# Performance work log

Hardware: AMD Instinct MI355X
Metric: run time of the kernel (lower is better)

## Reference

```python
import jax, jax.numpy as jnp
import numpy as np

N_LIG, N_PROT, K = 1024, 8192, 48
N = N_LIG + N_PROT
HID, FEAT, DEPTH = 256, 32, 5
NF = 6                      # sinusoid frequencies -> 12-dim distance embedding
EDGE_DIM = 4 * NF           # per-block dist emb (12) + top-level dist emb (12)
NORM = 5.0                  # agg_norm_factor
_FREQS = (2.0 * np.pi * 4.0 ** np.arange(NF) / 15.0).astype(np.float32)

def sin_emb(d2):
    # d2: [E,1] squared distances -> [E, 2*NF] sinusoidal embedding
    d = jnp.sqrt(d2 + 1e-8)
    x = d * _FREQS
    return jnp.concatenate([jnp.sin(x), jnp.cos(x)], axis=-1)

def knn_edges(coors):
    # KNN (k=48, no self loops) restricted to ligand query nodes (first N_LIG),
    # matching edges[:, :N_lig*k] slicing of knn_graph(flow='target_to_source').
    c = jax.lax.stop_gradient(coors)
    lig = c[:N_LIG]
    d2 = jnp.sum((lig[:, None, :] - c[None, :, :]) ** 2, axis=-1)  # [N_LIG, N]
    d2 = d2.at[jnp.arange(N_LIG), jnp.arange(N_LIG)].set(jnp.inf)
    _, idx = jax.lax.top_k(-d2, K)                                  # [N_LIG, K]
    row = jnp.repeat(jnp.arange(N_LIG), K)
    col = idx.reshape(-1)
    return row, col

def egnn(h, x, row, col, W_in, b_in, W_out, b_out, edge_W1, edge_b1, edge_W2, edge_b2, att_W, att_b, node_W1, node_b1, node_W2, node_b2, coord_W1, coord_b1, coord_W2, coord_b2, coord_W3):
    # EDM-style EGNN: per block 1 GCL (edge MLP + attention gate + node MLP residual)
    # followed by an equivariant coordinate update; sin distance embedding.
    emb0 = sin_emb(jnp.sum((x[row] - x[col]) ** 2, axis=-1, keepdims=True))
    h = h @ W_in + b_in
    for l in range(DEPTH):
        diff = x[row] - x[col]                         # [E,3]
        d2 = jnp.sum(diff ** 2, axis=-1, keepdims=True)
        cdiff = diff / (jnp.sqrt(d2 + 1e-8) + 1.0)     # norm_constant = 1
        ea = jnp.concatenate([sin_emb(d2), emb0], axis=-1)  # [E, EDGE_DIM]
        m = jax.nn.silu(jnp.concatenate([h[row], h[col], ea], axis=-1) @ edge_W1[l] + edge_b1[l])
        m = jax.nn.silu(m @ edge_W2[l] + edge_b2[l])
        m = m * jax.nn.sigmoid(m @ att_W[l] + att_b[l])         # attention gate
        agg = jax.ops.segment_sum(m, row, num_segments=N) / NORM
        u = jax.nn.silu(jnp.concatenate([h, agg], axis=-1) @ node_W1[l] + node_b1[l])
        h = h + (u @ node_W2[l] + node_b2[l])                    # residual node update
        c = jax.nn.silu(jnp.concatenate([h[row], h[col], ea], axis=-1) @ coord_W1[l] + coord_b1[l])  # use_latest_h
        c = jax.nn.silu(c @ coord_W2[l] + coord_b2[l])
        x = x + jax.ops.segment_sum(cdiff * (c @ coord_W3[l]), row, num_segments=N) / NORM
    return h @ W_out + b_out, x

def setup_inputs():
    key = jax.random.key(0)
    ks = jax.random.split(key, 24)
    f32 = jnp.float32
    def nrm(i, shape, scale=0.05):
        return jax.random.normal(ks[i], shape, dtype=f32) * scale
    return {
        'protein_positions': nrm(0, (N_PROT, 3), 3.0),
        'protein_ele': jax.random.randint(ks[1], (N_PROT,), 0, 5),
        'protein_amino_acid': jax.random.randint(ks[2], (N_PROT,), 0, 20),
        'protein_is_backbone': jax.random.randint(ks[3], (N_PROT,), 0, 2),
        'Xt_pos': nrm(4, (N_LIG, 3), 1.0),
        'Xt_features': nrm(5, (N_LIG, FEAT), 1.0),
        't': jax.random.randint(ks[6], (N_LIG,), 0, 1000),
        'Wt_time': nrm(7, (1000, 8), 1.0),
        'W_ele': nrm(8, (5, 16), 1.0),
        'W_aa': nrm(9, (20, 16), 1.0),
        'W_bb': nrm(10, (2, 8), 1.0),
        'W_in': nrm(11, (40, HID)), 'b_in': jnp.zeros((HID,), f32),
        'W_out': nrm(12, (HID, FEAT)), 'b_out': jnp.zeros((FEAT,), f32),
        'edge_W1': nrm(13, (DEPTH, 2 * HID + EDGE_DIM, HID)), 'edge_b1': jnp.zeros((DEPTH, HID), f32),
        'edge_W2': nrm(14, (DEPTH, HID, HID)), 'edge_b2': jnp.zeros((DEPTH, HID), f32),
        'att_W': nrm(15, (DEPTH, HID, 1)), 'att_b': jnp.zeros((DEPTH, 1), f32),
        'node_W1': nrm(16, (DEPTH, 2 * HID, HID)), 'node_b1': jnp.zeros((DEPTH, HID), f32),
        'node_W2': nrm(17, (DEPTH, HID, HID)), 'node_b2': jnp.zeros((DEPTH, HID), f32),
        'coord_W1': nrm(18, (DEPTH, 2 * HID + EDGE_DIM, HID)), 'coord_b1': jnp.zeros((DEPTH, HID), f32),
        'coord_W2': nrm(19, (DEPTH, HID, HID)), 'coord_b2': jnp.zeros((DEPTH, HID), f32),
        'coord_W3': nrm(20, (DEPTH, HID, 1), 0.001),
        'pos_w': jnp.ones((1, 1), f32),
    }

def reference(protein_positions, protein_ele, protein_amino_acid, protein_is_backbone, Xt_pos, Xt_features, t, Wt_time, W_ele, W_aa, W_bb, W_in, b_in, W_out, b_out, edge_W1, edge_b1, edge_W2, edge_b2, att_W, att_b, node_W1, node_b1, node_W2, node_b2, coord_W1, coord_b1, coord_W2, coord_b2, coord_W3, pos_w):
    prot_feat = jnp.concatenate([W_ele[protein_ele], W_aa[protein_amino_acid], W_bb[protein_is_backbone]], axis=-1)  # [N_PROT,40]
    feats = jnp.concatenate([jnp.concatenate([Xt_features, Wt_time[t]], axis=-1), prot_feat], axis=0)  # [N,40]
    coors = jnp.concatenate([Xt_pos, protein_positions], axis=0)  # [N,3]
    row, col = knn_edges(coors)
    h, x = egnn(feats, coors, row, col, W_in, b_in, W_out, b_out, edge_W1, edge_b1, edge_W2, edge_b2, att_W, att_b, node_W1, node_b1, node_W2, node_b2, coord_W1, coord_b1, coord_W2, coord_b2, coord_W3)
    # pos_linear: Linear(1,1,bias=False) applied elementwise == scalar multiply
    return x[:N_LIG] * pos_w[0, 0], h[:N_LIG]
```

## Files before the change

kernel.cpp:

```cpp
#include <hip/hip_runtime.h>
#include <hip/hip_bf16.h>
#include <math.h>

#define N_LIGC 1024
#define NTOT 9216
#define KNN 48
#define HID 256
#define DEPTHC 5
#define ETOT (N_LIGC*KNN)
#define KBINS 4096
#define PACK_BLKS 1484

typedef unsigned short u16;
typedef __attribute__((ext_vector_type(8))) short bf16x8;
typedef __attribute__((ext_vector_type(4))) float f32x4;

__device__ __forceinline__ float freq_f(int i){
  double p = (double)(1 << (2*i));
  return (float)((2.0*3.14159265358979323846)*p/15.0);
}
__device__ __forceinline__ float silu_f(float v){
  return v*__builtin_amdgcn_rcpf(1.0f+__expf(-v));
}
__device__ __forceinline__ float sigm_f(float v){
// ... 169 lines not shown
        aR[0][0]=__builtin_amdgcn_mfma_f32_16x16x32_bf16(a0,b0,aR[0][0],0,0,0);
        aR[0][1]=__builtin_amdgcn_mfma_f32_16x16x32_bf16(a0,b1,aR[0][1],0,0,0);
        aR[1][0]=__builtin_amdgcn_mfma_f32_16x16x32_bf16(a1,b0,aR[1][0],0,0,0);
        aR[1][1]=__builtin_amdgcn_mfma_f32_16x16x32_bf16(a1,b1,aR[1][1],0,0,0);
        aR[2][0]=__builtin_amdgcn_mfma_f32_16x16x32_bf16(a2,b0,aR[2][0],0,0,0);
        aR[2][1]=__builtin_amdgcn_mfma_f32_16x16x32_bf16(a2,b1,aR[2][1],0,0,0);
      }
      #pragma unroll
      for (int mt=0;mt<3;mt++)
      #pragma unroll
      for (int nt=0;nt<2;nt++){
        int n = wv*32 + nt*16 + nl;
        #pragma unroll
        for (int r=0;r<4;r++){
          int m = mt*16 + quad*4 + r;
          int node = base + m;
          if (m < 36 && node < N_LIGC) R[(size_t)node*HID + n] = aR[mt][nt][r];
        }
      }
    }
    return;
  }
  if (tid >= 256) return;
  unsigned int* hist  = (unsigned int*)smem;
  int*          candI = (int*)(smem + 16384);
  float*        candV = (float*)(smem + 20480);
  unsigned int* scanb = (unsigned int*)(smem + 24576);
  float*        selD  = (float*)(smem + 25600);
  int*          sInt  = (int*)(smem + 25792);
  int b = blockIdx.x - 256;
  for (int i=tid;i<KBINS;i+=256) hist[i]=0u;
  if (tid==0){ sInt[3]=0; }
  float px = X[b*3+0], py = X[b*3+1], pz = X[b*3+2];
  __syncthreads();
  float d2v[36];
  float mn = INFINITY;
  #pragma unroll
  for (int j=0;j<36;j++){
    int i = tid + 256*j;
    float dx = __fsub_rn(px, X[i*3+0]);
    float dy = __fsub_rn(py, X[i*3+1]);
    float dz = __fsub_rn(pz, X[i*3+2]);
    float d2 = __fadd_rn(__fadd_rn(__fmul_rn(dx,dx),__fmul_rn(dy,dy)),__fmul_rn(dz,dz));
    if (i==b) d2 = INFINITY;
    d2v[j] = d2;
    mn = fminf(mn, d2);
  }
  {
    unsigned mkey = __float_as_uint(mn) >> 19;
    if (mkey >= KBINS) mkey = KBINS-1;
    atomicAdd(&hist[mkey], 1u);
  }
  __syncthreads();
  unsigned s=0;
  {
    #pragma unroll 4
    for (int k=0;k<16;k++) s += hist[tid*16+k];
    scanb[tid]=s;
  }
  __syncthreads();
  #pragma unroll
  for (int off=1; off<256; off<<=1){
    unsigned v = (tid>=off) ? scanb[tid-off] : 0u;
    __syncthreads();
    scanb[tid] += v;
    __syncthreads();
  }
  {
    unsigned incl = scanb[tid];
    unsigned excl = incl - s;
    if (excl < (unsigned)KNN && incl >= (unsigned)KNN){ sInt[2] = tid; sInt[1] = (int)excl; }
  }
  __syncthreads();
  if (tid==0){
    unsigned c = (unsigned)sInt[1]; int bin = sInt[2]*16;
    for (;;bin++){
      unsigned hh = hist[bin];
      if (c + hh >= (unsigned)KNN) break;
      c += hh;
    }
    sInt[0] = bin;
  }
  __syncthreads();
  int Bp = sInt[0];
  #pragma unroll
  for (int j=0;j<36;j++){
    float d2 = d2v[j];
    int key = (int)(__float_as_uint(d2) >> 19);
    if (key <= Bp){
      int c = atomicAdd(&sInt[3], 1);
      if (c < 1024){ candI[c] = tid + 256*j; candV[c] = d2; }
    }
  }
  __syncthreads();
  {
    int m = sInt[3]; if (m > 1024) m = 1024;
    for (int c = tid; c < m; c += 256){
      float v = candV[c]; int idx = candI[c];
      int rank = 0;
      for (int o = 0; o < m; o++){
        float ov = candV[o];
        if (ov < v || (ov == v && candI[o] < idx)) rank++;
      }
      if (rank < KNN){ col[b*KNN+rank] = idx; selD[rank] = v; }
    }
  }
  __syncthreads();
  if (tid < KNN){
    float d = sqrtf(selD[tid] + 1e-8f);
    int base = (b*KNN+tid)*12;
    #pragma unroll
    for (int i=0;i<6;i++){
      float fr = freq_f(i);
      emb0[base+i]   = f2b_p(sinf(d*fr));
      emb0[base+6+i] = f2b_p(cosf(d*fr));
    }
  }
}

__global__ __launch_bounds__(256,4) void k_comb_edge(
    const u16* __restrict__ Qb, const float* __restrict__ R,
    const float* __restrict__ xc,
    const int* __restrict__ colIdx, const u16* __restrict__ emb0,
    const u16* __restrict__ W1cP, const float* __restrict__ B1,
    const u16* __restrict__ W2p, const float* __restrict__ B2,
    const float* __restrict__ attW, const float* __restrict__ attB,
    u16* __restrict__ agg_bf, int l)
{
  __shared__ __align__(16) u16 sQ[48*264];
  __shared__ __align__(16) u16 sEA[48*40];
  __shared__ float sR[256];
  __shared__ int sCol[48];
  __shared__ float sD[48];
  __shared__ float sSig[48];
  __shared__ float sDot[48][4];

  int row = blockIdx.x, tid = threadIdx.x;
  int lane = tid & 63, ng = tid >> 6;
  int quad = lane >> 4, nl = lane & 15;

  if (tid < 48) sCol[tid] = colIdx[(size_t)row*KNN + tid];
  sR[tid] = R[(size_t)row*HID + tid];
  __syncthreads();
  for (int t = tid; t < 48*32; t += 256){
    int e = t >> 5, q = t & 31;
    uint4 v = ((const uint4*)(Qb + (size_t)sCol[e]*HID))[q];
    *(uint4*)(sQ + e*264 + q*8) = v;
  }
  if (tid < 48){
    int cg = sCol[tid];
    float dx = xc[row*3+0]-xc[cg*3+0];
    float dy = xc[row*3+1]-xc[cg*3+1];
    float dz = xc[row*3+2]-xc[cg*3+2];
    float d = sqrtf(dx*dx+dy*dy+dz*dz + 1e-8f);
    sD[tid] = d;
    const unsigned int* ep = (const unsigned int*)(emb0 + ((size_t)row*KNN + tid)*12);
    unsigned int* dd = (unsigned int*)(sEA + tid*40 + 12);
    #pragma unroll
    for (int i=0;i<6;i++) dd[i] = ep[i];
    u16* ea = sEA + tid*40;
    #pragma unroll
    for (int i=24;i<32;i++) ea[i] = 0;
  }
  __syncthreads();
  for (int t=tid; t<288; t+=256){
    int e = t/6, i = t - 6*e;
    float fr = 0.41887903f * (float)(1 << (2*i));
    float x = sD[e]*fr;
    u16* ea = sEA + e*40;
    ea[i]   = f2b(__sinf(x));
    ea[6+i] = f2b(__cosf(x));
  }
  __syncthreads();

  f32x4 zero4 = {0.f,0.f,0.f,0.f};
  f32x4 acc[3][4];
  #pragma unroll
  for (int i=0;i<3;i++){ acc[i][0]=zero4; acc[i][1]=zero4; acc[i][2]=zero4; acc[i][3]=zero4; }
  {
    const u16* Wc = W1cP + (size_t)l*32*HID;
    const u16* wb = Wc + ((size_t)(ng*4)*64 + lane)*8;
    bf16x8 b0 = *(const bf16x8*)(wb);
    bf16x8 b1 = *(const bf16x8*)(wb + 512);
    bf16x8 b2 = *(const bf16x8*)(wb + 1024);
    bf16x8 b3 = *(const bf16x8*)(wb + 1536);
    bf16x8 a0 = *(const bf16x8*)(sEA + (0*16+nl)*40 + quad*8);
    bf16x8 a1 = *(const bf16x8*)(sEA + (1*16+nl)*40 + quad*8);
    bf16x8 a2 = *(const bf16x8*)(sEA + (2*16+nl)*40 + quad*8);
    acc[0][0]=__builtin_amdgcn_mfma_f32_16x16x32_bf16(a0,b0,acc[0][0],0,0,0);
    acc[0][1]=__builtin_amdgcn_mfma_f32_16x16x32_bf16(a0,b1,acc[0][1],0,0,0);
    acc[0][2]=__builtin_amdgcn_mfma_f32_16x16x32_bf16(a0,b2,acc[0][2],0,0,0);
    acc[0][3]=__builtin_amdgcn_mfma_f32_16x16x32_bf16(a0,b3,acc[0][3],0,0,0);
    acc[1][0]=__builtin_amdgcn_mfma_f32_16x16x32_bf16(a1,b0,acc[1][0],0,0,0);
    acc[1][1]=__builtin_amdgcn_mfma_f32_16x16x32_bf16(a1,b1,acc[1][1],0,0,0);
    acc[1][2]=__builtin_amdgcn_mfma_f32_16x16x32_bf16(a1,b2,acc[1][2],0,0,0);
    acc[1][3]=__builtin_amdgcn_mfma_f32_16x16x32_bf16(a1,b3,acc[1][3],0,0,0);
    acc[2][0]=__builtin_amdgcn_mfma_f32_16x16x32_bf16(a2,b0,acc[2][0],0,0,0);
    acc[2][1]=__builtin_amdgcn_mfma_f32_16x16x32_bf16(a2,b1,acc[2][1],0,0,0);
    acc[2][2]=__builtin_amdgcn_mfma_f32_16x16x32_bf16(a2,b2,acc[2][2],0,0,0);
    acc[2][3]=__builtin_amdgcn_mfma_f32_16x16x32_bf16(a2,b3,acc[2][3],0,0,0);
  }
  #pragma unroll
  for (int mt=0;mt<3;mt++)
  #pragma unroll
  for (int nt=0;nt<4;nt++){
    int n = ng*64 + nt*16 + nl;
    float bb = B1[l*HID + n] + sR[n];
    #pragma unroll
    for (int r=0;r<4;r++){
      int m = mt*16 + quad*4 + r;
      float v = acc[mt][nt][r] + bb + b2f(sQ[m*264 + n]);
      sQ[m*264 + n] = f2b(silu_f(v));
    }
  }
  __syncthreads();

  f32x4 acc2[3][4];
  #pragma unroll
  for (int i=0;i<3;i++){ acc2[i][0]=zero4; acc2[i][1]=zero4; acc2[i][2]=zero4; acc2[i][3]=zero4; }
  const u16* W2 = W2p + (size_t)l*HID*HID;
  #pragma unroll 2
  for (int k0=0;k0<8;k0++){
    bf16x8 a0 = *(const bf16x8*)(sQ + (0*16+nl)*264 + k0*32 + quad*8);
    bf16x8 a1 = *(const bf16x8*)(sQ + (1*16+nl)*264 + k0*32 + quad*8);
    bf16x8 a2 = *(const bf16x8*)(sQ + (2*16+nl)*264 + k0*32 + quad*8);
    const u16* wb = W2 + ((size_t)(k0*16 + ng*4)*64 + lane)*8;
    bf16x8 b0 = *(const bf16x8*)(wb);
    bf16x8 b1 = *(const bf16x8*)(wb + 512);
    bf16x8 b2 = *(const bf16x8*)(wb + 1024);
    bf16x8 b3 = *(const bf16x8*)(wb + 1536);
    acc2[0][0]=__builtin_amdgcn_mfma_f32_16x16x32_bf16(a0,b0,acc2[0][0],0,0,0);
    acc2[0][1]=__builtin_amdgcn_mfma_f32_16x16x32_bf16(a0,b1,acc2[0][1],0,0,0);
    acc2[0][2]=__builtin_amdgcn_mfma_f32_16x16x32_bf16(a0,b2,acc2[0][2],0,0,0);
    acc2[0][3]=__builtin_amdgcn_mfma_f32_16x16x32_bf16(a0,b3,acc2[0][3],0,0,0);
    acc2[1][0]=__builtin_amdgcn_mfma_f32_16x16x32_bf16(a1,b0,acc2[1][0],0,0,0);
    acc2[1][1]=__builtin_amdgcn_mfma_f32_16x16x32_bf16(a1,b1,acc2[1][1],0,0,0);
    acc2[1][2]=__builtin_amdgcn_mfma_f32_16x16x32_bf16(a1,b2,acc2[1][2],0,0,0);
    acc2[1][3]=__builtin_amdgcn_mfma_f32_16x16x32_bf16(a1,b3,acc2[1][3],0,0,0);
    acc2[2][0]=__builtin_amdgcn_mfma_f32_16x16x32_bf16(a2,b0,acc2[2][0],0,0,0);
    acc2[2][1]=__builtin_amdgcn_mfma_f32_16x16x32_bf16(a2,b1,acc2[2][1],0,0,0);
    acc2[2][2]=__builtin_amdgcn_mfma_f32_16x16x32_bf16(a2,b2,acc2[2][2],0,0,0);
    acc2[2][3]=__builtin_amdgcn_mfma_f32_16x16x32_bf16(a2,b3,acc2[2][3],0,0,0);
  }
  float aw[4], bb2[4];
  #pragma unroll
  for (int nt=0;nt<4;nt++){
    int n = ng*64 + nt*16 + nl;
    aw[nt]  = attW[l*HID + n];
    bb2[nt] = B2[l*HID + n];
  }
  float dotp[3][4];
  #pragma unroll
  for (int mt=0;mt<3;mt++){
    #pragma unroll
    for (int r=0;r<4;r++) dotp[mt][r] = 0.f;
    #pragma unroll
    for (int nt=0;nt<4;nt++){
      #pragma unroll
      for (int r=0;r<4;r++){
        float s = silu_f(acc2[mt][nt][r] + bb2[nt]);
        acc2[mt][nt][r] = s;
        dotp[mt][r] += s*aw[nt];
      }
    }
  }
  #pragma unroll
  for (int off=1; off<16; off<<=1){
    #pragma unroll
    for (int mt=0;mt<3;mt++)
    #pragma unroll
    for (int r=0;r<4;r++)
      dotp[mt][r] += __shfl_xor(dotp[mt][r], off);
  }
  if (nl == 0){
    #pragma unroll
    for (int mt=0;mt<3;mt++)
    #pragma unroll
    for (int r=0;r<4;r++)
      sDot[mt*16 + quad*4 + r][ng] = dotp[mt][r];
  }
  __syncthreads();
  if (tid < 48) sSig[tid] = sigm_f(sDot[tid][0]+sDot[tid][1]+sDot[tid][2]+sDot[tid][3] + attB[l]);
  __syncthreads();
  float sgv[3][4];
  #pragma unroll
  for (int mt=0;mt<3;mt++)
  #pragma unroll
  for (int r=0;r<4;r++)
    sgv[mt][r] = sSig[mt*16 + quad*4 + r];
  #pragma unroll
  for (int nt=0;nt<4;nt++){
    float a = 0.f;
    #pragma unroll
    for (int mt=0;mt<3;mt++)
    #pragma unroll
    for (int r=0;r<4;r++)
      a += acc2[mt][nt][r]*sgv[mt][r];
    a += __shfl_xor(a, 16);
    a += __shfl_xor(a, 32);
    if (quad == 0) agg_bf[(size_t)row*HID + ng*64 + nt*16 + nl] = f2b(a*0.2f);
  }
}

__global__ __launch_bounds__(512,1) void k_node(
    float* __restrict__ h,
    const u16* __restrict__ agg_bf,
    const u16* __restrict__ W1p, const float* __restrict__ B1,
    const u16* __restrict__ W2p, const float* __restrict__ B2,
    const u16* __restrict__ cWab, u16* __restrict__ QbC, float* __restrict__ RC,
    const u16* __restrict__ eWabN, u16* __restrict__ QbE, float* __restrict__ RE, int doE,
    const u16* __restrict__ WoutP, const float* __restrict__ bout,
    float* __restrict__ outH, int doOut, int l)
{
  __shared__ __align__(16) u16 sA[48*520];
  __shared__ __align__(16) u16 sU[48*264];
  u16* sH = sA;
  int blk=blockIdx.x, tid=threadIdx.x;
  int lane=tid&63, wv=tid>>6, quad=lane>>4, nl=lane&15;
  int base = blk*36;
  for (int t=tid; t<48*64; t+=512){
    int i=t>>6, s=t&63;
    unsigned int lo, hi;
    if (i < 36){
      float4 hv = ((const float4*)(h + (size_t)(base+i)*HID))[s];
      lo = (unsigned int)f2b(hv.x) | ((unsigned int)f2b(hv.y) << 16);
      hi = (unsigned int)f2b(hv.z) | ((unsigned int)f2b(hv.w) << 16);
    } else { lo = 0u; hi = 0u; }
    uint2 ov; ov.x = lo; ov.y = hi;
    *(uint2*)(sA + i*520 + s*4) = ov;
  }
  for (int t=tid; t<48*32; t+=512){
    int i=t>>5, q=t&31;
    uint4 v;
    int node = base+i;
    if (i < 36 && node < N_LIGC) v = ((const uint4*)(agg_bf + (size_t)node*HID))[q];
    else { v.x=0u; v.y=0u; v.z=0u; v.w=0u; }
    *(uint4*)(sA + i*520 + 256 + q*8) = v;
  }
  __syncthreads();
  f32x4 zero4 = {0.f,0.f,0.f,0.f};
  f32x4 acc[3][2];
  #pragma unroll
  for (int i=0;i<3;i++){ acc[i][0]=zero4; acc[i][1]=zero4; }
  const u16* Wp = W1p + (size_t)l*512*HID;
  #pragma unroll 2
  for (int k0=0;k0<16;k0++){
    bf16x8 a0 = *(const bf16x8*)(sA + (0*16+nl)*520 + k0*32 + quad*8);
    bf16x8 a1 = *(const bf16x8*)(sA + (1*16+nl)*520 + k0*32 + quad*8);
    bf16x8 a2 = *(const bf16x8*)(sA + (2*16+nl)*520 + k0*32 + quad*8);
    const u16* wb = Wp + ((size_t)(k0*16 + wv*2)*64 + lane)*8;
    bf16x8 b0 = *(const bf16x8*)(wb);
    bf16x8 b1 = *(const bf16x8*)(wb + 512);
    acc[0][0]=__builtin_amdgcn_mfma_f32_16x16x32_bf16(a0,b0,acc[0][0],0,0,0);
    acc[0][1]=__builtin_amdgcn_mfma_f32_16x16x32_bf16(a0,b1,acc[0][1],0,0,0);
    acc[1][0]=__builtin_amdgcn_mfma_f32_16x16x32_bf16(a1,b0,acc[1][0],0,0,0);
    acc[1][1]=__builtin_amdgcn_mfma_f32_16x16x32_bf16(a1,b1,acc[1][1],0,0,0);
    acc[2][0]=__builtin_amdgcn_mfma_f32_16x16x32_bf16(a2,b0,acc[2][0],0,0,0);
    acc[2][1]=__builtin_amdgcn_mfma_f32_16x16x32_bf16(a2,b1,acc[2][1],0,0,0);
  }
  #pragma unroll
  for (int mt=0;mt<3;mt++)
  #pragma unroll
  for (int nt=0;nt<2;nt++){
    int n = wv*32 + nt*16 + nl;
    float bb = B1[l*HID + n];
    #pragma unroll
    for (int r=0;r<4;r++){
      int m = mt*16 + quad*4 + r;
      sU[m*264 + n] = f2b(silu_f(acc[mt][nt][r] + bb));
    }
  }
  __syncthreads();
  f32x4 acc2[3][2];
  #pragma unroll
  for (int i=0;i<3;i++){ acc2[i][0]=zero4; acc2[i][1]=zero4; }
  const u16* W2 = W2p + (size_t)l*HID*HID;
  #pragma unroll 2
  for (int k0=0;k0<8;k0++){
    bf16x8 a0 = *(const bf16x8*)(sU + (0*16+nl)*264 + k0*32 + quad*8);
    bf16x8 a1 = *(const bf16x8*)(sU + (1*16+nl)*264 + k0*32 + quad*8);
    bf16x8 a2 = *(const bf16x8*)(sU + (2*16+nl)*264 + k0*32 + quad*8);
    const u16* wb = W2 + ((size_t)(k0*16 + wv*2)*64 + lane)*8;
    bf16x8 b0 = *(const bf16x8*)(wb);
    bf16x8 b1 = *(const bf16x8*)(wb + 512);
    acc2[0][0]=__builtin_amdgcn_mfma_f32_16x16x32_bf16(a0,b0,acc2[0][0],0,0,0);
    acc2[0][1]=__builtin_amdgcn_mfma_f32_16x16x32_bf16(a0,b1,acc2[0][1],0,0,0);
    acc2[1][0]=__builtin_amdgcn_mfma_f32_16x16x32_bf16(a1,b0,acc2[1][0],0,0,0);
    acc2[1][1]=__builtin_amdgcn_mfma_f32_16x16x32_bf16(a1,b1,acc2[1][1],0,0,0);
    acc2[2][0]=__builtin_amdgcn_mfma_f32_16x16x32_bf16(a2,b0,acc2[2][0],0,0,0);
    acc2[2][1]=__builtin_amdgcn_mfma_f32_16x16x32_bf16(a2,b1,acc2[2][1],0,0,0);
  }
  #pragma unroll
  for (int mt=0;mt<3;mt++)
  #pragma unroll
  for (int nt=0;nt<2;nt++){
    int n = wv*32 + nt*16 + nl;
    float bb = B2[l*HID + n];
    #pragma unroll
    for (int r=0;r<4;r++){
      int m = mt*16 + quad*4 + r;
      if (m < 36){
        size_t idx = (size_t)(base+m)*HID + n;
        float v = h[idx] + acc2[mt][nt][r] + bb;
        h[idx] = v;
        sH[m*264 + n] = f2b(v);
      } else {
        sH[m*264 + n] = 0;
      }
    }
  }
  __syncthreads();

  int isLig = (base < N_LIGC);
  const u16* Wl = cWab + (size_t)l*512*HID;
  {
    f32x4 qc[3][2], qe[3][2];
    #pragma unroll
    for (int i=0;i<3;i++){ qc[i][0]=zero4; qc[i][1]=zero4; qe[i][0]=zero4; qe[i][1]=zero4; }
    #pragma unroll 2
    for (int k0=0;k0<8;k0++){
      bf16x8 a0 = *(const bf16x8*)(sH + (0*16+nl)*264 + k0*32 + quad*8);
      bf16x8 a1 = *(const bf16x8*)(sH + (1*16+nl)*264 + k0*32 + quad*8);
      bf16x8 a2 = *(const bf16x8*)(sH + (2*16+nl)*264 + k0*32 + quad*8);
      const u16* wbC = Wl    + ((size_t)((k0+8)*16 + wv*2)*64 + lane)*8;
      const u16* wbE = eWabN + ((size_t)((k0+8)*16 + wv*2)*64 + lane)*8;
      bf16x8 c0 = *(const bf16x8*)(wbC);
      bf16x8 c1 = *(const bf16x8*)(wbC + 512);
      bf16x8 e0 = *(const bf16x8*)(wbE);
      bf16x8 e1 = *(const bf16x8*)(wbE + 512);
      qc[0][0]=__builtin_amdgcn_mfma_f32_16x16x32_bf16(a0,c0,qc[0][0],0,0,0);
      qc[0][1]=__builtin_amdgcn_mfma_f32_16x16x32_bf16(a0,c1,qc[0][1],0,0,0);
      qc[1][0]=__builtin_amdgcn_mfma_f32_16x16x32_bf16(a1,c0,qc[1][0],0,0,0);
      qc[1][1]=__builtin_amdgcn_mfma_f32_16x16x32_bf16(a1,c1,qc[1][1],0,0,0);
      qc[2][0]=__builtin_amdgcn_mfma_f32_16x16x32_bf16(a2,c0,qc[2][0],0,0,0);
      qc[2][1]=__builtin_amdgcn_mfma_f32_16x16x32_bf16(a2,c1,qc[2][1],0,0,0);
      qe[0][0]=__builtin_amdgcn_mfma_f32_16x16x32_bf16(a0,e0,qe[0][0],0,0,0);
      qe[0][1]=__builtin_amdgcn_mfma_f32_16x16x32_bf16(a0,e1,qe[0][1],0,0,0);
      qe[1][0]=__builtin_amdgcn_mfma_f32_16x16x32_bf16(a1,e0,qe[1][0],0,0,0);
      qe[1][1]=__builtin_amdgcn_mfma_f32_16x16x32_bf16(a1,e1,qe[1][1],0,0,0);
      qe[2][0]=__builtin_amdgcn_mfma_f32_16x16x32_bf16(a2,e0,qe[2][0],0,0,0);
      qe[2][1]=__builtin_amdgcn_mfma_f32_16x16x32_bf16(a2,e1,qe[2][1],0,0,0);
    }
    #pragma unroll
    for (int mt=0;mt<3;mt++)
    #pragma unroll
    for (int nt=0;nt<2;nt++){
      int n = wv*32 + nt*16 + nl;
      #pragma unroll
      for (int r=0;r<4;r++){
        int m = mt*16 + quad*4 + r;
        if (m < 36) QbC[(size_t)(base+m)*HID + n] = f2b(qc[mt][nt][r]);
      }
    }
    if (doE){
      #pragma unroll
      for (int mt=0;mt<3;mt++)
      #pragma unroll
      for (int nt=0;nt<2;nt++){
        int n = wv*32 + nt*16 + nl;
        #pragma unroll
        for (int r=0;r<4;r++){
          int m = mt*16 + quad*4 + r;
          if (m < 36) QbE[(size_t)(base+m)*HID + n] = f2b(qe[mt][nt][r]);
        }
      }
    }
  }
  if (isLig){
    f32x4 rc[3][2], re[3][2];
    #pragma unroll
    for (int i=0;i<3;i++){ rc[i][0]=zero4; rc[i][1]=zero4; re[i][0]=zero4; re[i][1]=zero4; }
    #pragma unroll 2
    for (int k0=0;k0<8;k0++){
      bf16x8 a0 = *(const bf16x8*)(sH + (0*16+nl)*264 + k0*32 + quad*8);
      bf16x8 a1 = *(const bf16x8*)(sH + (1*16+nl)*264 + k0*32 + quad*8);
      bf16x8 a2 = *(const bf16x8*)(sH + (2*16+nl)*264 + k0*32 + quad*8);
      const u16* wbC = Wl    + ((size_t)(k0*16 + wv*2)*64 + lane)*8;
      const u16* wbE = eWabN + ((size_t)(k0*16 + wv*2)*64 + lane)*8;
      bf16x8 c0 = *(const bf16x8*)(wbC);
      bf16x8 c1 = *(const bf16x8*)(wbC + 512);
      bf16x8 e0 = *(const bf16x8*)(wbE);
      bf16x8 e1 = *(const bf16x8*)(wbE + 512);
      rc[0][0]=__builtin_amdgcn_mfma_f32_16x16x32_bf16(a0,c0,rc[0][0],0,0,0);
      rc[0][1]=__builtin_amdgcn_mfma_f32_16x16x32_bf16(a0,c1,rc[0][1],0,0,0);
      rc[1][0]=__builtin_amdgcn_mfma_f32_16x16x32_bf16(a1,c0,rc[1][0],0,0,0);
      rc[1][1]=__builtin_amdgcn_mfma_f32_16x16x32_bf16(a1,c1,rc[1][1],0,0,0);
      rc[2][0]=__builtin_amdgcn_mfma_f32_16x16x32_bf16(a2,c0,rc[2][0],0,0,0);
      rc[2][1]=__builtin_amdgcn_mfma_f32_16x16x32_bf16(a2,c1,rc[2][1],0,0,0);
      re[0][0]=__builtin_amdgcn_mfma_f32_16x16x32_bf16(a0,e0,re[0][0],0,0,0);
      re[0][1]=__builtin_amdgcn_mfma_f32_16x16x32_bf16(a0,e1,re[0][1],0,0,0);
      re[1][0]=__builtin_amdgcn_mfma_f32_16x16x32_bf16(a1,e0,re[1][0],0,0,0);
      re[1][1]=__builtin_amdgcn_mfma_f32_16x16x32_bf16(a1,e1,re[1][1],0,0,0);
      re[2][0]=__builtin_amdgcn_mfma_f32_16x16x32_bf16(a2,e0,re[2][0],0,0,0);
      re[2][1]=__builtin_amdgcn_mfma_f32_16x16x32_bf16(a2,e1,re[2][1],0,0,0);
    }
    #pragma unroll
    for (int mt=0;mt<3;mt++)
    #pragma unroll
    for (int nt=0;nt<2;nt++){
      int n = wv*32 + nt*16 + nl;
      #pragma unroll
      for (int r=0;r<4;r++){
        int m = mt*16 + quad*4 + r;
        int node = base + m;
        if (m < 36 && node < N_LIGC) RC[(size_t)node*HID + n] = rc[mt][nt][r];
      }
    }
    if (doE){
      #pragma unroll
      for (int mt=0;mt<3;mt++)
      #pragma unroll
      for (int nt=0;nt<2;nt++){
        int n = wv*32 + nt*16 + nl;
        #pragma unroll
        for (int r=0;r<4;r++){
          int m = mt*16 + quad*4 + r;
          int node = base + m;
          if (m < 36 && node < N_LIGC) RE[(size_t)node*HID + n] = re[mt][nt][r];
        }
      }
    }
  }
  if (doOut && isLig && wv < 2){
    int ntw = wv;
    f32x4 o[3]; o[0]=zero4; o[1]=zero4; o[2]=zero4;
    #pragma unroll 2
    for (int k0=0;k0<8;k0++){
      bf16x8 b = *(const bf16x8*)(WoutP + ((size_t)(k0*2 + ntw)*64 + lane)*8);
      #pragma unroll
      for (int mt=0;mt<3;mt++){
        bf16x8 a = *(const bf16x8*)(sH + (mt*16+nl)*264 + k0*32 + quad*8);
        o[mt] = __builtin_amdgcn_mfma_f32_16x16x32_bf16(a,b,o[mt],0,0,0);
      }
    }
    int n = ntw*16 + nl;
    float bb = bout[n];
    #pragma unroll
    for (int mt=0;mt<3;mt++)
    #pragma unroll
    for (int r=0;r<4;r++){
      int m = mt*16 + quad*4 + r;
      int node = base + m;
      if (m < 36 && node < N_LIGC)
        outH[(size_t)node*32 + n] = o[mt][r] + bb;
    }
  }
}

__global__ __launch_bounds__(256,4) void k_comb_coord(
    const u16* __restrict__ Qb, const float* __restrict__ R,
    const float* __restrict__ xc, float* __restrict__ xn,
    const int* __restrict__ colIdx, const u16* __restrict__ emb0,
    const u16* __restrict__ W1cP, const float* __restrict__ B1,
    const u16* __restrict__ W2p, const float* __restrict__ B2,
    const float* __restrict__ cW3,
    const float* __restrict__ posw, float* __restrict__ outX, int doOut, int l)
{
  __shared__ __align__(16) u16 sQ[48*264];
  __shared__ __align__(16) u16 sEA[48*40];
  __shared__ float sR[256];
  __shared__ int sCol[48];
  __shared__ float sD[48];
  __shared__ float sCd[48*3];
  __shared__ float sS[48];
  __shared__ float sDot[48][4];

  int row = blockIdx.x, tid = threadIdx.x;
  int lane = tid & 63, ng = tid >> 6;
  int quad = lane >> 4, nl = lane & 15;

  if (tid < 48) sCol[tid] = colIdx[(size_t)row*KNN + tid];
  sR[tid] = R[(size_t)row*HID + tid];
  __syncthreads();
  for (int t = tid; t < 48*32; t += 256){
    int e = t >> 5, q = t & 31;
    uint4 v = ((const uint4*)(Qb + (size_t)sCol[e]*HID))[q];
    *(uint4*)(sQ + e*264 + q*8) = v;
  }
  if (tid < 48){
    int cg = sCol[tid];
    float dx = xc[row*3+0]-xc[cg*3+0];
    float dy = xc[row*3+1]-xc[cg*3+1];
    float dz = xc[row*3+2]-xc[cg*3+2];
    float d = sqrtf(dx*dx+dy*dy+dz*dz + 1e-8f);
    sD[tid] = d;
    float rden = __builtin_amdgcn_rcpf(d + 1.0f);
    sCd[tid*3+0]=dx*rden; sCd[tid*3+1]=dy*rden; sCd[tid*3+2]=dz*rden;
    const unsigned int* ep = (const unsigned int*)(emb0 + ((size_t)row*KNN + tid)*12);
    unsigned int* dd = (unsigned int*)(sEA + tid*40 + 12);
    #pragma unroll
    for (int i=0;i<6;i++) dd[i] = ep[i];
    u16* ea = sEA + tid*40;
    #pragma unroll
    for (int i=24;i<32;i++) ea[i] = 0;
  }
  __syncthreads();
  for (int t=tid; t<288; t+=256){
    int e = t/6, i = t - 6*e;
    float fr = 0.41887903f * (float)(1 << (2*i));
    float x = sD[e]*fr;
    u16* ea = sEA + e*40;
    ea[i]   = f2b(__sinf(x));
    ea[6+i] = f2b(__cosf(x));
  }
  __syncthreads();

  f32x4 zero4 = {0.f,0.f,0.f,0.f};
  f32x4 acc[3][4];
  #pragma unroll
  for (int i=0;i<3;i++){ acc[i][0]=zero4; acc[i][1]=zero4; acc[i][2]=zero4; acc[i][3]=zero4; }
  {
    const u16* Wc = W1cP + (size_t)l*32*HID;
    const u16* wb = Wc + ((size_t)(ng*4)*64 + lane)*8;
    bf16x8 b0 = *(const bf16x8*)(wb);
    bf16x8 b1 = *(const bf16x8*)(wb + 512);
    bf16x8 b2 = *(const bf16x8*)(wb + 1024);
    bf16x8 b3 = *(const bf16x8*)(wb + 1536);
    bf16x8 a0 = *(const bf16x8*)(sEA + (0*16+nl)*40 + quad*8);
    bf16x8 a1 = *(const bf16x8*)(sEA + (1*16+nl)*40 + quad*8);
    bf16x8 a2 = *(const bf16x8*)(sEA + (2*16+nl)*40 + quad*8);
    acc[0][0]=__builtin_amdgcn_mfma_f32_16x16x32_bf16(a0,b0,acc[0][0],0,0,0);
    acc[0][1]=__builtin_amdgcn_mfma_f32_16x16x32_bf16(a0,b1,acc[0][1],0,0,0);
    acc[0][2]=__builtin_amdgcn_mfma_f32_16x16x32_bf16(a0,b2,acc[0][2],0,0,0);
    acc[0][3]=__builtin_amdgcn_mfma_f32_16x16x32_bf16(a0,b3,acc[0][3],0,0,0);
    acc[1][0]=__builtin_amdgcn_mfma_f32_16x16x32_bf16(a1,b0,acc[1][0],0,0,0);
    acc[1][1]=__builtin_amdgcn_mfma_f32_16x16x32_bf16(a1,b1,acc[1][1],0,0,0);
    acc[1][2]=__builtin_amdgcn_mfma_f32_16x16x32_bf16(a1,b2,acc[1][2],0,0,0);
    acc[1][3]=__builtin_amdgcn_mfma_f32_16x16x32_bf16(a1,b3,acc[1][3],0,0,0);
    acc[2][0]=__builtin_amdgcn_mfma_f32_16x16x32_bf16(a2,b0,acc[2][0],0,0,0);
    acc[2][1]=__builtin_amdgcn_mfma_f32_16x16x32_bf16(a2,b1,acc[2][1],0,0,0);
    acc[2][2]=__builtin_amdgcn_mfma_f32_16x16x32_bf16(a2,b2,acc[2][2],0,0,0);
    acc[2][3]=__builtin_amdgcn_mfma_f32_16x16x32_bf16(a2,b3,acc[2][3],0,0,0);
  }
  #pragma unroll
  for (int mt=0;mt<3;mt++)
  #pragma unroll
  for (int nt=0;nt<4;nt++){
    int n = ng*64 + nt*16 + nl;
    float bb = B1[l*HID + n] + sR[n];
    #pragma unroll
    for (int r=0;r<4;r++){
      int m = mt*16 + quad*4 + r;
      float v = acc[mt][nt][r] + bb + b2f(sQ[m*264 + n]);
      sQ[m*264 + n] = f2b(silu_f(v));
    }
  }
  __syncthreads();

  f32x4 acc2[3][4];
  #pragma unroll
  for (int i=0;i<3;i++){ acc2[i][0]=zero4; acc2[i][1]=zero4; acc2[i][2]=zero4; acc2[i][3]=zero4; }
  const u16* W2 = W2p + (size_t)l*HID*HID;
  #pragma unroll 2
  for (int k0=0;k0<8;k0++){
    bf16x8 a0 = *(const bf16x8*)(sQ + (0*16+nl)*264 + k0*32 + quad*8);
    bf16x8 a1 = *(const bf16x8*)(sQ + (1*16+nl)*264 + k0*32 + quad*8);
    bf16x8 a2 = *(const bf16x8*)(sQ + (2*16+nl)*264 + k0*32 + quad*8);
    const u16* wb = W2 + ((size_t)(k0*16 + ng*4)*64 + lane)*8;
    bf16x8 b0 = *(const bf16x8*)(wb);
    bf16x8 b1 = *(const bf16x8*)(wb + 512);
    bf16x8 b2 = *(const bf16x8*)(wb + 1024);
    bf16x8 b3 = *(const bf16x8*)(wb + 1536);
    acc2[0][0]=__builtin_amdgcn_mfma_f32_16x16x32_bf16(a0,b0,acc2[0][0],0,0,0);
    acc2[0][1]=__builtin_amdgcn_mfma_f32_16x16x32_bf16(a0,b1,acc2[0][1],0,0,0);
    acc2[0][2]=__builtin_amdgcn_mfma_f32_16x16x32_bf16(a0,b2,acc2[0][2],0,0,0);
    acc2[0][3]=__builtin_amdgcn_mfma_f32_16x16x32_bf16(a0,b3,acc2[0][3],0,0,0);
    acc2[1][0]=__builtin_amdgcn_mfma_f32_16x16x32_bf16(a1,b0,acc2[1][0],0,0,0);
    acc2[1][1]=__builtin_amdgcn_mfma_f32_16x16x32_bf16(a1,b1,acc2[1][1],0,0,0);
    acc2[1][2]=__builtin_amdgcn_mfma_f32_16x16x32_bf16(a1,b2,acc2[1][2],0,0,0);
    acc2[1][3]=__builtin_amdgcn_mfma_f32_16x16x32_bf16(a1,b3,acc2[1][3],0,0,0);
    acc2[2][0]=__builtin_amdgcn_mfma_f32_16x16x32_bf16(a2,b0,acc2[2][0],0,0,0);
    acc2[2][1]=__builtin_amdgcn_mfma_f32_16x16x32_bf16(a2,b1,acc2[2][1],0,0,0);
    acc2[2][2]=__builtin_amdgcn_mfma_f32_16x16x32_bf16(a2,b2,acc2[2][2],0,0,0);
    acc2[2][3]=__builtin_amdgcn_mfma_f32_16x16x32_bf16(a2,b3,acc2[2][3],0,0,0);
  }
  float cw[4], bb2[4];
  #pragma unroll
  for (int nt=0;nt<4;nt++){
    int n = ng*64 + nt*16 + nl;
    cw[nt]  = cW3[l*HID + n];
    bb2[nt] = B2[l*HID + n];
  }
  float dotp[3][4];
  #pragma unroll
  for (int mt=0;mt<3;mt++){
    #pragma unroll
    for (int r=0;r<4;r++) dotp[mt][r] = 0.f;
    #pragma unroll
    for (int nt=0;nt<4;nt++){
      #pragma unroll
      for (int r=0;r<4;r++){
        float s = silu_f(acc2[mt][nt][r] + bb2[nt]);
        dotp[mt][r] += s*cw[nt];
      }
    }
  }
  #pragma unroll
  for (int off=1; off<16; off<<=1){
    #pragma unroll
    for (int mt=0;mt<3;mt++)
    #pragma unroll
    for (int r=0;r<4;r++)
      dotp[mt][r] += __shfl_xor(dotp[mt][r], off);
  }
  if (nl == 0){
    #pragma unroll
    for (int mt=0;mt<3;mt++)
    #pragma unroll
    for (int r=0;r<4;r++)
      sDot[mt*16 + quad*4 + r][ng] = dotp[mt][r];
  }
  __syncthreads();
  if (tid < 48) sS[tid] = sDot[tid][0]+sDot[tid][1]+sDot[tid][2]+sDot[tid][3];
  __syncthreads();
  if (tid < 3){
    float u = 0.f;
    #pragma unroll 4
    for (int e=0;e<48;e++) u += sCd[e*3+tid]*sS[e];
    float nv = xc[row*3+tid] + u*0.2f;
    xn[row*3+tid] = nv;
    if (doOut) outX[row*3+tid] = nv*posw[0];
  }
}

extern "C" void kernel_launch(void* const* d_in, const int* in_sizes, int n_in,
                              void* d_out, int out_size, void* d_ws, size_t ws_size,
                              hipStream_t stream)
{
  const float* protPos = (const float*)d_in[0];
  const int*   protEle = (const int*)d_in[1];
  const int*   protAA  = (const int*)d_in[2];
  const int*   protBB  = (const int*)d_in[3];
  const float* XtPos   = (const float*)d_in[4];
  const float* XtFeat  = (const float*)d_in[5];
  const int*   tArr    = (const int*)d_in[6];
  const float* WtTime  = (const float*)d_in[7];
  const float* Wele    = (const float*)d_in[8];
  const float* Waa     = (const float*)d_in[9];
  const float* Wbb     = (const float*)d_in[10];
  const float* Win     = (const float*)d_in[11];
  const float* bin     = (const float*)d_in[12];
  const float* Wout    = (const float*)d_in[13];
  const float* bout    = (const float*)d_in[14];
  const float* eW1     = (const float*)d_in[15];
  const float* eB1     = (const float*)d_in[16];
  const float* eW2     = (const float*)d_in[17];
  const float* eB2     = (const float*)d_in[18];
  const float* attW    = (const float*)d_in[19];
  const float* attB    = (const float*)d_in[20];
  const float* nW1     = (const float*)d_in[21];
  const float* nB1     = (const float*)d_in[22];
  const float* nW2     = (const float*)d_in[23];
  const float* nB2     = (const float*)d_in[24];
  const float* cW1     = (const float*)d_in[25];
  const float* cB1     = (const float*)d_in[26];
  const float* cW2     = (const float*)d_in[27];
  const float* cB2     = (const float*)d_in[28];
  const float* cW3     = (const float*)d_in[29];
  const float* posw    = (const float*)d_in[30];

  float* fp = (float*)d_ws;
  float* X0   = fp;               fp += NTOT*3;
  float* X1   = fp;               fp += NTOT*3;
  float* h    = fp;               fp += (size_t)NTOT*HID;
  float* RC   = fp;               fp += (size_t)N_LIGC*HID;
  float* RE   = fp;               fp += (size_t)N_LIGC*HID;
  int*   col  = (int*)fp;         fp += ETOT;
  u16*   up   = (u16*)fp;
  u16* emb0   = up;               up += (size_t)ETOT*12;
  u16* h_bf   = up;               up += (size_t)NTOT*HID;
  u16* agg_bf = up;               up += (size_t)N_LIGC*HID;
  u16* QbE    = up;               up += (size_t)NTOT*HID;
  u16* QbC    = up;               up += (size_t)NTOT*HID;
  u16* eW1abP = up;               up += (size_t)DEPTHC*512*HID;
  u16* eW1cP  = up;               up += (size_t)DEPTHC*32*HID;
  u16* eW2p   = up;               up += (size_t)DEPTHC*HID*HID;
  u16* nW1p   = up;               up += (size_t)DEPTHC*512*HID;
  u16* nW2p   = up;               up += (size_t)DEPTHC*HID*HID;
  u16* cW1abP = up;               up += (size_t)DEPTHC*512*HID;
  u16* cW1cP  = up;               up += (size_t)DEPTHC*32*HID;
  u16* cW2p   = up;               up += (size_t)DEPTHC*HID*HID;
  u16* WoutP  = up;               up += (size_t)256*32;

  k_prep<<<PACK_BLKS + NTOT/8,256,0,stream>>>(eW1,eW2,nW1,nW2,cW1,cW2,Wout,
      eW1abP,eW1cP,eW2p,nW1p,nW2p,cW1abP,cW1cP,cW2p,WoutP,
      protPos,protEle,protAA,protBB,XtPos,XtFeat,
      tArr,WtTime,Wele,Waa,Wbb,Win,bin,X0,X1,h,h_bf);
  k_knn_pq<<<256 + N_LIGC,512,0,stream>>>(X0,col,emb0,h_bf,eW1abP,RE,QbE);

  float* xc = X0; float* xn = X1;
  float* outF = (float*)d_out;
  for (int l=0;l<DEPTHC;l++){
    k_comb_edge<<<N_LIGC,256,0,stream>>>(QbE,RE,xc,col,emb0,eW1cP,eB1,eW2p,eB2,attW,attB,agg_bf,l);
    const u16* eNext = eW1abP + (size_t)((l+1)%DEPTHC)*512*HID;
    k_node<<<256,512,0,stream>>>(h,agg_bf,nW1p,nB1,nW2p,nB2,
        cW1abP,QbC,RC, eNext,QbE,RE,(l<DEPTHC-1)?1:0,
        WoutP,bout, outF+3072, (l==DEPTHC-1)?1:0, l);
    k_comb_coord<<<N_LIGC,256,0,stream>>>(QbC,RC,xc,xn,col,emb0,cW1cP,cB1,cW2p,cB2,cW3,
        posw, outF, (l==DEPTHC-1)?1:0, l);
    float* t2=xc; xc=xn; xn=t2;
  }
}
```

Measured before the change: 478.2 us.

## Double k_node block to 1024 threads with one 16-column tile per wave

Raises the node-MLP kernel from 8 to 16 waves per block. Each wave now owns a single 16-wide output column tile instead of two, which halves per-wave accumulators and weight loads and deepens the unroll. The goal is more latency hiding and more concurrent MFMA work inside the 256-block grid. In exchange it doubles wave count per CU and may raise register and scheduling pressure, with the same LDS footprint per block.

```diff
diff --git a/kernel.cpp b/kernel.cpp
--- a/kernel.cpp
+++ b/kernel.cpp
@@ -495,7 +495,7 @@
   }
 }
 
-__global__ __launch_bounds__(512,1) void k_node(
+__global__ __launch_bounds__(1024,1) void k_node(
     float* __restrict__ h,
     const u16* __restrict__ agg_bf,
     const u16* __restrict__ W1p, const float* __restrict__ B1,
@@ -511,7 +511,7 @@
   int blk=blockIdx.x, tid=threadIdx.x;
   int lane=tid&63, wv=tid>>6, quad=lane>>4, nl=lane&15;
   int base = blk*36;
-  for (int t=tid; t<48*64; t+=512){
+  for (int t=tid; t<48*64; t+=1024){
     int i=t>>6, s=t&63;
     unsigned int lo, hi;
     if (i < 36){
@@ -522,7 +522,7 @@
     uint2 ov; ov.x = lo; ov.y = hi;
     *(uint2*)(sA + i*520 + s*4) = ov;
   }
-  for (int t=tid; t<48*32; t+=512){
+  for (int t=tid; t<48*32; t+=1024){
     int i=t>>5, q=t&31;
     uint4 v;
     int node = base+i;
@@ -532,69 +532,54 @@
   }
   __syncthreads();
   f32x4 zero4 = {0.f,0.f,0.f,0.f};
-  f32x4 acc[3][2];
-  #pragma unroll
-  for (int i=0;i<3;i++){ acc[i][0]=zero4; acc[i][1]=zero4; }
+  int n = wv*16 + nl;
+  f32x4 acc[3];
+  acc[0]=zero4; acc[1]=zero4; acc[2]=zero4;
   const u16* Wp = W1p + (size_t)l*512*HID;
-  #pragma unroll 2
+  #pragma unroll 4
   for (int k0=0;k0<16;k0++){
     bf16x8 a0 = *(const bf16x8*)(sA + (0*16+nl)*520 + k0*32 + quad*8);
     bf16x8 a1 = *(const bf16x8*)(sA + (1*16+nl)*520 + k0*32 + quad*8);
     bf16x8 a2 = *(const bf16x8*)(sA + (2*16+nl)*520 + k0*32 + quad*8);
-    const u16* wb = Wp + ((size_t)(k0*16 + wv*2)*64 + lane)*8;
-    bf16x8 b0 = *(const bf16x8*)(wb);
-    bf16x8 b1 = *(const bf16x8*)(wb + 512);
-    acc[0][0]=__builtin_amdgcn_mfma_f32_16x16x32_bf16(a0,b0,acc[0][0],0,0,0);
-    acc[0][1]=__builtin_amdgcn_mfma_f32_16x16x32_bf16(a0,b1,acc[0][1],0,0,0);
-    acc[1][0]=__builtin_amdgcn_mfma_f32_16x16x32_bf16(a1,b0,acc[1][0],0,0,0);
-    acc[1][1]=__builtin_amdgcn_mfma_f32_16x16x32_bf16(a1,b1,acc[1][1],0,0,0);
-    acc[2][0]=__builtin_amdgcn_mfma_f32_16x16x32_bf16(a2,b0,acc[2][0],0,0,0);
-    acc[2][1]=__builtin_amdgcn_mfma_f32_16x16x32_bf16(a2,b1,acc[2][1],0,0,0);
-  }
-  #pragma unroll
-  for (int mt=0;mt<3;mt++)
-  #pragma unroll
-  for (int nt=0;nt<2;nt++){
-    int n = wv*32 + nt*16 + nl;
+    bf16x8 b0 = *(const bf16x8*)(Wp + ((size_t)(k0*16 + wv)*64 + lane)*8);
+    acc[0]=__builtin_amdgcn_mfma_f32_16x16x32_bf16(a0,b0,acc[0],0,0,0);
+    acc[1]=__builtin_amdgcn_mfma_f32_16x16x32_bf16(a1,b0,acc[1],0,0,0);
+    acc[2]=__builtin_amdgcn_mfma_f32_16x16x32_bf16(a2,b0,acc[2],0,0,0);
+  }
+  {
     float bb = B1[l*HID + n];
+    #pragma unroll
+    for (int mt=0;mt<3;mt++)
     #pragma unroll
     for (int r=0;r<4;r++){
       int m = mt*16 + quad*4 + r;
-      sU[m*264 + n] = f2b(silu_f(acc[mt][nt][r] + bb));
-    }
-  }
-  __syncthreads();
-  f32x4 acc2[3][2];
-  #pragma unroll
-  for (int i=0;i<3;i++){ acc2[i][0]=zero4; acc2[i][1]=zero4; }
+      sU[m*264 + n] = f2b(silu_f(acc[mt][r] + bb));
+    }
+  }
+  __syncthreads();
+  f32x4 acc2[3];
+  acc2[0]=zero4; acc2[1]=zero4; acc2[2]=zero4;
   const u16* W2 = W2p + (size_t)l*HID*HID;
-  #pragma unroll 2
+  #pragma unroll 4
   for (int k0=0;k0<8;k0++){
     bf16x8 a0 = *(const bf16x8*)(sU + (0*16+nl)*264 + k0*32 + quad*8);
     bf16x8 a1 = *(const bf16x8*)(sU + (1*16+nl)*264 + k0*32 + quad*8);
     bf16x8 a2 = *(const bf16x8*)(sU + (2*16+nl)*264 + k0*32 + quad*8);
-    const u16* wb = W2 + ((size_t)(k0*16 + wv*2)*64 + lane)*8;
-    bf16x8 b0 = *(const bf16x8*)(wb);
-    bf16x8 b1 = *(const bf16x8*)(wb + 512);
-    acc2[0][0]=__builtin_amdgcn_mfma_f32_16x16x32_bf16(a0,b0,acc2[0][0],0,0,0);
-    acc2[0][1]=__builtin_amdgcn_mfma_f32_16x16x32_bf16(a0,b1,acc2[0][1],0,0,0);
-    acc2[1][0]=__builtin_amdgcn_mfma_f32_16x16x32_bf16(a1,b0,acc2[1][0],0,0,0);
-    acc2[1][1]=__builtin_amdgcn_mfma_f32_16x16x32_bf16(a1,b1,acc2[1][1],0,0,0);
-    acc2[2][0]=__builtin_amdgcn_mfma_f32_16x16x32_bf16(a2,b0,acc2[2][0],0,0,0);
-    acc2[2][1]=__builtin_amdgcn_mfma_f32_16x16x32_bf16(a2,b1,acc2[2][1],0,0,0);
-  }
-  #pragma unroll
-  for (int mt=0;mt<3;mt++)
-  #pragma unroll
-  for (int nt=0;nt<2;nt++){
-    int n = wv*32 + nt*16 + nl;
+    bf16x8 b0 = *(const bf16x8*)(W2 + ((size_t)(k0*16 + wv)*64 + lane)*8);
+    acc2[0]=__builtin_amdgcn_mfma_f32_16x16x32_bf16(a0,b0,acc2[0],0,0,0);
+    acc2[1]=__builtin_amdgcn_mfma_f32_16x16x32_bf16(a1,b0,acc2[1],0,0,0);
+    acc2[2]=__builtin_amdgcn_mfma_f32_16x16x32_bf16(a2,b0,acc2[2],0,0,0);
+  }
+  {
     float bb = B2[l*HID + n];
+    #pragma unroll
+    for (int mt=0;mt<3;mt++)
     #pragma unroll
     for (int r=0;r<4;r++){
       int m = mt*16 + quad*4 + r;
       if (m < 36){
         size_t idx = (size_t)(base+m)*HID + n;
-        float v = h[idx] + acc2[mt][nt][r] + bb;
+        float v = h[idx] + acc2[mt][r] + bb;
         h[idx] = v;
         sH[m*264 + n] = f2b(v);
       } else {
@@ -607,110 +592,74 @@
   int isLig = (base < N_LIGC);
   const u16* Wl = cWab + (size_t)l*512*HID;
   {
-    f32x4 qc[3][2], qe[3][2];
-    #pragma unroll
-    for (int i=0;i<3;i++){ qc[i][0]=zero4; qc[i][1]=zero4; qe[i][0]=zero4; qe[i][1]=zero4; }
-    #pragma unroll 2
+    f32x4 qc[3], qe[3];
+    qc[0]=zero4; qc[1]=zero4; qc[2]=zero4;
+    qe[0]=zero4; qe[1]=zero4; qe[2]=zero4;
+    #pragma unroll 4
     for (int k0=0;k0<8;k0++){
       bf16x8 a0 = *(const bf16x8*)(sH + (0*16+nl)*264 + k0*32 + quad*8);
       bf16x8 a1 = *(const bf16x8*)(sH + (1*16+nl)*264 + k0*32 + quad*8);
       bf16x8 a2 = *(const bf16x8*)(sH + (2*16+nl)*264 + k0*32 + quad*8);
-      const u16* wbC = Wl    + ((size_t)((k0+8)*16 + wv*2)*64 + lane)*8;
-      const u16* wbE = eWabN + ((size_t)((k0+8)*16 + wv*2)*64 + lane)*8;
-      bf16x8 c0 = *(const bf16x8*)(wbC);
-      bf16x8 c1 = *(const bf16x8*)(wbC + 512);
-      bf16x8 e0 = *(const bf16x8*)(wbE);
-      bf16x8 e1 = *(const bf16x8*)(wbE + 512);
-      qc[0][0]=__builtin_amdgcn_mfma_f32_16x16x32_bf16(a0,c0,qc[0][0],0,0,0);
-      qc[0][1]=__builtin_amdgcn_mfma_f32_16x16x32_bf16(a0,c1,qc[0][1],0,0,0);
-      qc[1][0]=__builtin_amdgcn_mfma_f32_16x16x32_bf16(a1,c0,qc[1][0],0,0,0);
-      qc[1][1]=__builtin_amdgcn_mfma_f32_16x16x32_bf16(a1,c1,qc[1][1],0,0,0);
-      qc[2][0]=__builtin_amdgcn_mfma_f32_16x16x32_bf16(a2,c0,qc[2][0],0,0,0);
-      qc[2][1]=__builtin_amdgcn_mfma_f32_16x16x32_bf16(a2,c1,qc[2][1],0,0,0);
-      qe[0][0]=__builtin_amdgcn_mfma_f32_16x16x32_bf16(a0,e0,qe[0][0],0,0,0);
-      qe[0][1]=__builtin_amdgcn_mfma_f32_16x16x32_bf16(a0,e1,qe[0][1],0,0,0);
-      qe[1][0]=__builtin_amdgcn_mfma_f32_16x16x32_bf16(a1,e0,qe[1][0],0,0,0);
-      qe[1][1]=__builtin_amdgcn_mfma_f32_16x16x32_bf16(a1,e1,qe[1][1],0,0,0);
-      qe[2][0]=__builtin_amdgcn_mfma_f32_16x16x32_bf16(a2,e0,qe[2][0],0,0,0);
-      qe[2][1]=__builtin_amdgcn_mfma_f32_16x16x32_bf16(a2,e1,qe[2][1],0,0,0);
-    }
-    #pragma unroll
-    for (int mt=0;mt<3;mt++)
-    #pragma unroll
-    for (int nt=0;nt<2;nt++){
-      int n = wv*32 + nt*16 + nl;
+      bf16x8 c0 = *(const bf16x8*)(Wl    + ((size_t)((k0+8)*16 + wv)*64 + lane)*8);
+      bf16x8 e0 = *(const bf16x8*)(eWabN + ((size_t)((k0+8)*16 + wv)*64 + lane)*8);
+      qc[0]=__builtin_amdgcn_mfma_f32_16x16x32_bf16(a0,c0,qc[0],0,0,0);
+      qc[1]=__builtin_amdgcn_mfma_f32_16x16x32_bf16(a1,c0,qc[1],0,0,0);
+      qc[2]=__builtin_amdgcn_mfma_f32_16x16x32_bf16(a2,c0,qc[2],0,0,0);
+      qe[0]=__builtin_amdgcn_mfma_f32_16x16x32_bf16(a0,e0,qe[0],0,0,0);
+      qe[1]=__builtin_amdgcn_mfma_f32_16x16x32_bf16(a1,e0,qe[1],0,0,0);
+      qe[2]=__builtin_amdgcn_mfma_f32_16x16x32_bf16(a2,e0,qe[2],0,0,0);
+    }
+    #pragma unroll
+    for (int mt=0;mt<3;mt++)
+    #pragma unroll
+    for (int r=0;r<4;r++){
+      int m = mt*16 + quad*4 + r;
+      if (m < 36) QbC[(size_t)(base+m)*HID + n] = f2b(qc[mt][r]);
+    }
+    if (doE){
+      #pragma unroll
+      for (int mt=0;mt<3;mt++)
       #pragma unroll
       for (int r=0;r<4;r++){
         int m = mt*16 + quad*4 + r;
-        if (m < 36) QbC[(size_t)(base+m)*HID + n] = f2b(qc[mt][nt][r]);
-      }
-    }
-    if (doE){
-      #pragma unroll
-      for (int mt=0;mt<3;mt++)
-      #pragma unroll
-      for (int nt=0;nt<2;nt++){
-        int n = wv*32 + nt*16 + nl;
-        #pragma unroll
-        for (int r=0;r<4;r++){
-          int m = mt*16 + quad*4 + r;
-          if (m < 36) QbE[(size_t)(base+m)*HID + n] = f2b(qe[mt][nt][r]);
-        }
+        if (m < 36) QbE[(size_t)(base+m)*HID + n] = f2b(qe[mt][r]);
       }
     }
   }
   if (isLig){
-    f32x4 rc[3][2], re[3][2];
-    #pragma unroll
-    for (int i=0;i<3;i++){ rc[i][0]=zero4; rc[i][1]=zero4; re[i][0]=zero4; re[i][1]=zero4; }
-    #pragma unroll 2
+    f32x4 rc[3], re[3];
+    rc[0]=zero4; rc[1]=zero4; rc[2]=zero4;
+    re[0]=zero4; re[1]=zero4; re[2]=zero4;
+    #pragma unroll 4
     for (int k0=0;k0<8;k0++){
       bf16x8 a0 = *(const bf16x8*)(sH + (0*16+nl)*264 + k0*32 + quad*8);
       bf16x8 a1 = *(const bf16x8*)(sH + (1*16+nl)*264 + k0*32 + quad*8);
       bf16x8 a2 = *(const bf16x8*)(sH + (2*16+nl)*264 + k0*32 + quad*8);
-      const u16* wbC = Wl    + ((size_t)(k0*16 + wv*2)*64 + lane)*8;
-      const u16* wbE = eWabN + ((size_t)(k0*16 + wv*2)*64 + lane)*8;
-      bf16x8 c0 = *(const bf16x8*)(wbC);
-      bf16x8 c1 = *(const bf16x8*)(wbC + 512);
-      bf16x8 e0 = *(const bf16x8*)(wbE);
-      bf16x8 e1 = *(const bf16x8*)(wbE + 512);
-      rc[0][0]=__builtin_amdgcn_mfma_f32_16x16x32_bf16(a0,c0,rc[0][0],0,0,0);
-      rc[0][1]=__builtin_amdgcn_mfma_f32_16x16x32_bf16(a0,c1,rc[0][1],0,0,0);
-      rc[1][0]=__builtin_amdgcn_mfma_f32_16x16x32_bf16(a1,c0,rc[1][0],0,0,0);
-      rc[1][1]=__builtin_amdgcn_mfma_f32_16x16x32_bf16(a1,c1,rc[1][1],0,0,0);
-      rc[2][0]=__builtin_amdgcn_mfma_f32_16x16x32_bf16(a2,c0,rc[2][0],0,0,0);
-      rc[2][1]=__builtin_amdgcn_mfma_f32_16x16x32_bf16(a2,c1,rc[2][1],0,0,0);
-      re[0][0]=__builtin_amdgcn_mfma_f32_16x16x32_bf16(a0,e0,re[0][0],0,0,0);
-      re[0][1]=__builtin_amdgcn_mfma_f32_16x16x32_bf16(a0,e1,re[0][1],0,0,0);
-      re[1][0]=__builtin_amdgcn_mfma_f32_16x16x32_bf16(a1,e0,re[1][0],0,0,0);
-      re[1][1]=__builtin_amdgcn_mfma_f32_16x16x32_bf16(a1,e1,re[1][1],0,0,0);
-      re[2][0]=__builtin_amdgcn_mfma_f32_16x16x32_bf16(a2,e0,re[2][0],0,0,0);
-      re[2][1]=__builtin_amdgcn_mfma_f32_16x16x32_bf16(a2,e1,re[2][1],0,0,0);
-    }
-    #pragma unroll
-    for (int mt=0;mt<3;mt++)
-    #pragma unroll
-    for (int nt=0;nt<2;nt++){
-      int n = wv*32 + nt*16 + nl;
+      bf16x8 c0 = *(const bf16x8*)(Wl    + ((size_t)(k0*16 + wv)*64 + lane)*8);
+      bf16x8 e0 = *(const bf16x8*)(eWabN + ((size_t)(k0*16 + wv)*64 + lane)*8);
+      rc[0]=__builtin_amdgcn_mfma_f32_16x16x32_bf16(a0,c0,rc[0],0,0,0);
+      rc[1]=__builtin_amdgcn_mfma_f32_16x16x32_bf16(a1,c0,rc[1],0,0,0);
+      rc[2]=__builtin_amdgcn_mfma_f32_16x16x32_bf16(a2,c0,rc[2],0,0,0);
+      re[0]=__builtin_amdgcn_mfma_f32_16x16x32_bf16(a0,e0,re[0],0,0,0);
+      re[1]=__builtin_amdgcn_mfma_f32_16x16x32_bf16(a1,e0,re[1],0,0,0);
+      re[2]=__builtin_amdgcn_mfma_f32_16x16x32_bf16(a2,e0,re[2],0,0,0);
+    }
+    #pragma unroll
+    for (int mt=0;mt<3;mt++)
+    #pragma unroll
+    for (int r=0;r<4;r++){
+      int m = mt*16 + quad*4 + r;
+      int node = base + m;
+      if (m < 36 && node < N_LIGC) RC[(size_t)node*HID + n] = rc[mt][r];
+    }
+    if (doE){
+      #pragma unroll
+      for (int mt=0;mt<3;mt++)
       #pragma unroll
       for (int r=0;r<4;r++){
         int m = mt*16 + quad*4 + r;
         int node = base + m;
-        if (m < 36 && node < N_LIGC) RC[(size_t)node*HID + n] = rc[mt][nt][r];
-      }
-    }
-    if (doE){
-      #pragma unroll
-      for (int mt=0;mt<3;mt++)
-      #pragma unroll
-      for (int nt=0;nt<2;nt++){
-        int n = wv*32 + nt*16 + nl;
-        #pragma unroll
-        for (int r=0;r<4;r++){
-          int m = mt*16 + quad*4 + r;
-          int node = base + m;
-          if (m < 36 && node < N_LIGC) RE[(size_t)node*HID + n] = re[mt][nt][r];
-        }
+        if (m < 36 && node < N_LIGC) RE[(size_t)node*HID + n] = re[mt][r];
       }
     }
   }
@@ -726,8 +675,8 @@
         o[mt] = __builtin_amdgcn_mfma_f32_16x16x32_bf16(a,b,o[mt],0,0,0);
       }
     }
-    int n = ntw*16 + nl;
-    float bb = bout[n];
+    int no = ntw*16 + nl;
+    float bb = bout[no];
     #pragma unroll
     for (int mt=0;mt<3;mt++)
     #pragma unroll
@@ -735,7 +684,7 @@
       int m = mt*16 + quad*4 + r;
       int node = base + m;
       if (m < 36 && node < N_LIGC)
-        outH[(size_t)node*32 + n] = o[mt][r] + bb;
+        outH[(size_t)node*32 + no] = o[mt][r] + bb;
     }
   }
 }
@@ -986,7 +935,7 @@
   for (int l=0;l<DEPTHC;l++){
     k_comb_edge<<<N_LIGC,256,0,stream>>>(QbE,RE,xc,col,emb0,eW1cP,eB1,eW2p,eB2,attW,attB,agg_bf,l);
     const u16* eNext = eW1abP + (size_t)((l+1)%DEPTHC)*512*HID;
-    k_node<<<256,512,0,stream>>>(h,agg_bf,nW1p,nB1,nW2p,nB2,
+    k_node<<<256,1024,0,stream>>>(h,agg_bf,nW1p,nB1,nW2p,nB2,
         cW1abP,QbC,RC, eNext,QbE,RE,(l<DEPTHC-1)?1:0,
         WoutP,bout, outF+3072, (l==DEPTHC-1)?1:0, l);
     k_comb_coord<<<N_LIGC,256,0,stream>>>(QbC,RC,xc,xn,col,emb0,cW1cP,cB1,cW2p,cB2,cW3,
```

New measurement: 463.1 us, median of 2. 1.03x faster.
